# Optimization experiments

Hardware: AMD Instinct MI355X
Metric: run time of the kernel (lower is better)

## Reference

```python
import jax, jax.numpy as jnp
import numpy as np

B, S, D = 32768, 16, 64


def setup_inputs() -> dict:
    key = jax.random.key(0)
    k1, k2, k3, k4 = jax.random.split(key, 4)
    z1 = jax.random.normal(k1, (B, S, D), dtype=jnp.float32)
    z2 = jax.random.normal(k2, (B, S, D), dtype=jnp.float32)
    a = jax.random.uniform(k3, (), dtype=jnp.float32)          # constrained to [0,1]
    b = jax.random.normal(k4, (), dtype=jnp.float32)
    return {"z1": z1, "z2": z2, "a": a, "b": b}


def reference(z1, z2, a, b):
    # Pairwise Euclidean distances between the S MC samples of z1 and z2
    # per batch element: dist[b, i, j] = ||z1[b,i] - z2[b,j]||_2.
    sq1 = jnp.sum(z1 * z1, axis=-1)                    # [B, S]
    sq2 = jnp.sum(z2 * z2, axis=-1)                    # [B, S]
    dots = jnp.einsum('bid,bjd->bij', z1, z2)          # [B, S, S]
    d2 = sq1[:, :, None] + sq2[:, None, :] - 2.0 * dots
    dist = jnp.sqrt(jnp.maximum(d2, 0.0))              # [B, S, S]
    # Original concatenates over samples -> [B, S*S] (then squeeze).
    dist = dist.reshape(dist.shape[0], -1)             # [B, S*S]
    logit = jax.nn.sigmoid(dist * a + b)
    return jnp.clip(logit, 1e-08, 1.0)
```

## Files before the change

kernel.cpp:

```cpp
#include <hip/hip_runtime.h>
#include <hip/hip_bf16.h>
#include <math.h>

#define Bn 32768
#define Sn 16
#define Dn 64
#define NB 2
#define SSTR 72
#define THREADS 128

typedef __attribute__((ext_vector_type(8))) unsigned short ushort8v;
typedef __attribute__((ext_vector_type(4))) unsigned short ushort4v;

static __device__ inline unsigned short f2bf(float f) {
    __hip_bfloat16 h = __float2bfloat16(f);
    return *reinterpret_cast<unsigned short*>(&h);
}
static __device__ inline float bf2f(unsigned short u) {
    union { unsigned int i; float f; } v;
    v.i = ((unsigned int)u) << 16;
    return v.f;
}

__global__ __launch_bounds__(THREADS, 8)
void get_logit_mc_kernel(const float* __restrict__ z1,
                         const float* __restrict__ z2,
                         const float* __restrict__ pa,
                         const float* __restrict__ pb,
                         float* __restrict__ out) {
    __shared__ __align__(16) unsigned short zs[2][NB][Sn][SSTR];

    const int t  = threadIdx.x;
    const int bb = blockIdx.x * NB;

    #pragma unroll
    for (int k = 0; k < 8; ++k) {
        int Q     = t + k * THREADS;
        int batch = Q >> 9;
        int arr   = (Q >> 8) & 1;
        int row   = (Q >> 4) & 15;
        int q     = Q & 15;
        const float* src = (arr ? z2 : z1) +
            (((size_t)(bb + batch) * Sn + row) * Dn + q * 4);
        float4 v = *reinterpret_cast<const float4*>(src);
        ushort4v w;
        w.x = f2bf(v.x); w.y = f2bf(v.y); w.z = f2bf(v.z); w.w = f2bf(v.w);
        *reinterpret_cast<ushort4v*>(&zs[arr][batch][row][q * 4]) = w;
    }

    const float av = pa[0];
    const float bv = pb[0];

    __syncthreads();

    const int bl = t >> 6;
    const int r  = (t >> 3) & 7;
    const int c  = t & 7;

    float acc[2][2] = {{0.f,0.f},{0.f,0.f}};

    #pragma unroll
    for (int qq = 0; qq < 8; ++qq) {
        ushort8v x0 = *reinterpret_cast<const ushort8v*>(&zs[0][bl][2*r    ][qq*8]);
        ushort8v x1 = *reinterpret_cast<const ushort8v*>(&zs[0][bl][2*r + 1][qq*8]);
        ushort8v y0 = *reinterpret_cast<const ushort8v*>(&zs[1][bl][2*c    ][qq*8]);
        ushort8v y1 = *reinterpret_cast<const ushort8v*>(&zs[1][bl][2*c + 1][qq*8]);
        #pragma unroll
        for (int e = 0; e < 8; ++e) {
            float a0 = bf2f(x0[e]);
            float a1 = bf2f(x1[e]);
            float b0 = bf2f(y0[e]);
            float b1 = bf2f(y1[e]);
            float d;
            d = a0 - b0; acc[0][0] = fmaf(d, d, acc[0][0]);
            d = a0 - b1; acc[0][1] = fmaf(d, d, acc[0][1]);
            d = a1 - b0; acc[1][0] = fmaf(d, d, acc[1][0]);
            d = a1 - b1; acc[1][1] = fmaf(d, d, acc[1][1]);
        }
    }

    #pragma unroll
    for (int ii = 0; ii < 2; ++ii) {
        float2 o;
        #pragma unroll
        for (int jj = 0; jj < 2; ++jj) {
            float dist = sqrtf(acc[ii][jj]);
            float x    = fmaf(dist, av, bv);
            float e    = __expf(-x);
            float sg   = 1.0f / (1.0f + e);
            sg = fminf(sg, 1.0f);
            sg = fmaxf(sg, 1e-8f);
            (&o.x)[jj] = sg;
        }
        int i = 2*r + ii;
        float* dst = out + ((size_t)(bb + bl) * (Sn * Sn) + i * Sn + c * 2);
        *reinterpret_cast<float2*>(dst) = o;
    }
}

extern "C" void kernel_launch(void* const* d_in, const int* in_sizes, int n_in,
                              void* d_out, int out_size, void* d_ws, size_t ws_size,
                              hipStream_t stream) {
    const float* z1 = (const float*)d_in[0];
    const float* z2 = (const float*)d_in[1];
    const float* pa = (const float*)d_in[2];
    const float* pb = (const float*)d_in[3];
    float* out      = (float*)d_out;

    dim3 grid(Bn / NB);
    dim3 block(THREADS);
    hipLaunchKernelGGL(get_logit_mc_kernel, grid, block, 0, stream,
                       z1, z2, pa, pb, out);
}
```

Baseline: 57.22 us.

## Compute pairwise distances with bf16 MFMA dot products, one wave per batch

Replaces the LDS-staged scalar difference-of-squares loop with a Gram-matrix formulation. Each wave loads one batch's rows directly into registers as bf16 fragments and runs two 16x16x32 bf16 MFMAs to get the dot products. Row norms come from lane-local sums reduced with shuffles. This drops shared memory and __syncthreads and moves the arithmetic onto matrix cores. The cost is possible cancellation error in ||a||^2+||b||^2-2ab, which is clamped at zero.

```diff
diff --git a/kernel.cpp b/kernel.cpp
--- a/kernel.cpp
+++ b/kernel.cpp
@@ -5,12 +5,11 @@
 #define Bn 32768
 #define Sn 16
 #define Dn 64
-#define NB 2
-#define SSTR 72
-#define THREADS 128
+#define THREADS 256
+#define WPB 4
 
-typedef __attribute__((ext_vector_type(8))) unsigned short ushort8v;
-typedef __attribute__((ext_vector_type(4))) unsigned short ushort4v;
+typedef __attribute__((ext_vector_type(8))) short bf16x8;
+typedef __attribute__((ext_vector_type(4))) float f32x4;
 
 static __device__ inline unsigned short f2bf(float f) {
     __hip_bfloat16 h = __float2bfloat16(f);
@@ -22,79 +21,84 @@
     return v.f;
 }
 
-__global__ __launch_bounds__(THREADS, 8)
+static __device__ inline bf16x8 cvt_frag(float4 lo, float4 hi, float& s) {
+    bf16x8 r;
+    const float* pl = &lo.x;
+    const float* ph = &hi.x;
+    #pragma unroll
+    for (int j = 0; j < 4; ++j) {
+        unsigned short u = f2bf(pl[j]);
+        float f = bf2f(u);
+        s = fmaf(f, f, s);
+        r[j] = (short)u;
+    }
+    #pragma unroll
+    for (int j = 0; j < 4; ++j) {
+        unsigned short u = f2bf(ph[j]);
+        float f = bf2f(u);
+        s = fmaf(f, f, s);
+        r[4 + j] = (short)u;
+    }
+    return r;
+}
+
+__global__ __launch_bounds__(THREADS, 4)
 void get_logit_mc_kernel(const float* __restrict__ z1,
                          const float* __restrict__ z2,
                          const float* __restrict__ pa,
                          const float* __restrict__ pb,
                          float* __restrict__ out) {
-    __shared__ __align__(16) unsigned short zs[2][NB][Sn][SSTR];
+    const int t     = threadIdx.x;
+    const int wave  = t >> 6;
+    const int lane  = t & 63;
+    const int batch = blockIdx.x * WPB + wave;
+    const int m     = lane & 15;
+    const int g     = lane >> 4;
 
-    const int t  = threadIdx.x;
-    const int bb = blockIdx.x * NB;
+    const float* p1 = z1 + ((size_t)batch << 10) + (m << 6);
+    const float* p2 = z2 + ((size_t)batch << 10) + (m << 6);
 
-    #pragma unroll
-    for (int k = 0; k < 8; ++k) {
-        int Q     = t + k * THREADS;
-        int batch = Q >> 9;
-        int arr   = (Q >> 8) & 1;
-        int row   = (Q >> 4) & 15;
-        int q     = Q & 15;
-        const float* src = (arr ? z2 : z1) +
-            (((size_t)(bb + batch) * Sn + row) * Dn + q * 4);
-        float4 v = *reinterpret_cast<const float4*>(src);
-        ushort4v w;
-        w.x = f2bf(v.x); w.y = f2bf(v.y); w.z = f2bf(v.z); w.w = f2bf(v.w);
-        *reinterpret_cast<ushort4v*>(&zs[arr][batch][row][q * 4]) = w;
-    }
+    float4 a0 = *reinterpret_cast<const float4*>(p1 + g * 8);
+    float4 a1 = *reinterpret_cast<const float4*>(p1 + g * 8 + 4);
+    float4 a2 = *reinterpret_cast<const float4*>(p1 + 32 + g * 8);
+    float4 a3 = *reinterpret_cast<const float4*>(p1 + 32 + g * 8 + 4);
+    float4 b0 = *reinterpret_cast<const float4*>(p2 + g * 8);
+    float4 b1 = *reinterpret_cast<const float4*>(p2 + g * 8 + 4);
+    float4 b2 = *reinterpret_cast<const float4*>(p2 + 32 + g * 8);
+    float4 b3 = *reinterpret_cast<const float4*>(p2 + 32 + g * 8 + 4);
+
+    float s1 = 0.0f, s2 = 0.0f;
+    bf16x8 fa0 = cvt_frag(a0, a1, s1);
+    bf16x8 fa1 = cvt_frag(a2, a3, s1);
+    bf16x8 fb0 = cvt_frag(b0, b1, s2);
+    bf16x8 fb1 = cvt_frag(b2, b3, s2);
+
+    f32x4 acc = {0.f, 0.f, 0.f, 0.f};
+    acc = __builtin_amdgcn_mfma_f32_16x16x32_bf16(fa0, fb0, acc, 0, 0, 0);
+    acc = __builtin_amdgcn_mfma_f32_16x16x32_bf16(fa1, fb1, acc, 0, 0, 0);
+
+    s1 += __shfl_xor(s1, 16);
+    s1 += __shfl_xor(s1, 32);
+    s2 += __shfl_xor(s2, 16);
+    s2 += __shfl_xor(s2, 32);
 
     const float av = pa[0];
     const float bv = pb[0];
 
-    __syncthreads();
-
-    const int bl = t >> 6;
-    const int r  = (t >> 3) & 7;
-    const int c  = t & 7;
-
-    float acc[2][2] = {{0.f,0.f},{0.f,0.f}};
-
+    float* po = out + ((size_t)batch << 8);
     #pragma unroll
-    for (int qq = 0; qq < 8; ++qq) {
-        ushort8v x0 = *reinterpret_cast<const ushort8v*>(&zs[0][bl][2*r    ][qq*8]);
-        ushort8v x1 = *reinterpret_cast<const ushort8v*>(&zs[0][bl][2*r + 1][qq*8]);
-        ushort8v y0 = *reinterpret_cast<const ushort8v*>(&zs[1][bl][2*c    ][qq*8]);
-        ushort8v y1 = *reinterpret_cast<const ushort8v*>(&zs[1][bl][2*c + 1][qq*8]);
-        #pragma unroll
-        for (int e = 0; e < 8; ++e) {
-            float a0 = bf2f(x0[e]);
-            float a1 = bf2f(x1[e]);
-            float b0 = bf2f(y0[e]);
-            float b1 = bf2f(y1[e]);
-            float d;
-            d = a0 - b0; acc[0][0] = fmaf(d, d, acc[0][0]);
-            d = a0 - b1; acc[0][1] = fmaf(d, d, acc[0][1]);
-            d = a1 - b0; acc[1][0] = fmaf(d, d, acc[1][0]);
-            d = a1 - b1; acc[1][1] = fmaf(d, d, acc[1][1]);
-        }
-    }
-
-    #pragma unroll
-    for (int ii = 0; ii < 2; ++ii) {
-        float2 o;
-        #pragma unroll
-        for (int jj = 0; jj < 2; ++jj) {
-            float dist = sqrtf(acc[ii][jj]);
-            float x    = fmaf(dist, av, bv);
-            float e    = __expf(-x);
-            float sg   = 1.0f / (1.0f + e);
-            sg = fminf(sg, 1.0f);
-            sg = fmaxf(sg, 1e-8f);
-            (&o.x)[jj] = sg;
-        }
-        int i = 2*r + ii;
-        float* dst = out + ((size_t)(bb + bl) * (Sn * Sn) + i * Sn + c * 2);
-        *reinterpret_cast<float2*>(dst) = o;
+    for (int j = 0; j < 4; ++j) {
+        int   row = g * 4 + j;
+        float s1r = __shfl(s1, row);
+        float d2  = s1r + s2 - 2.0f * acc[j];
+        d2 = fmaxf(d2, 0.0f);
+        float dist = sqrtf(d2);
+        float x    = fmaf(dist, av, bv);
+        float e    = __expf(-x);
+        float sg   = 1.0f / (1.0f + e);
+        sg = fminf(sg, 1.0f);
+        sg = fmaxf(sg, 1e-8f);
+        po[row * 16 + m] = sg;
     }
 }
 
@@ -107,7 +111,7 @@
     const float* pb = (const float*)d_in[3];
     float* out      = (float*)d_out;
 
-    dim3 grid(Bn / NB);
+    dim3 grid(Bn / WPB);
     dim3 block(THREADS);
     hipLaunchKernelGGL(get_logit_mc_kernel, grid, block, 0, stream,
                        z1, z2, pa, pb, out);
```

After: 49.70 us (median of 2 runs). 13.1% less time.
